# Performance work log

Hardware: AMD Instinct MI355X
Metric: run time of the kernel (lower is better)

The kernel has to match this reference:

```python
import jax, jax.numpy as jnp
import numpy as np

N, E, D, H, HOPS, HEAD_DIM = 50000, 800000, 256, 8, 2, 32


def setup_inputs() -> dict:
    key = jax.random.key(0)
    ks = jax.random.split(key, 9)
    scale = 1.0 / np.sqrt(D)  # mimic nn.Linear init scale
    return {
        "node_features": jax.random.normal(ks[0], (N, D), dtype=jnp.float32),
        "Wh_w": jax.random.normal(ks[1], (H, D, D), dtype=jnp.float32) * scale,
        "Wh_b": jax.random.normal(ks[2], (H, D), dtype=jnp.float32) * scale,
        "Wp_w": jax.random.normal(ks[3], (H, HEAD_DIM, D), dtype=jnp.float32) * scale,
        "Wp_b": jax.random.normal(ks[4], (H, HEAD_DIM), dtype=jnp.float32) * scale,
        "gate_vector": jax.random.normal(ks[5], (H,), dtype=jnp.float32),
        "hop_weights": jax.random.normal(ks[6], (HOPS,), dtype=jnp.float32),
        "src": jax.random.randint(ks[7], (E,), 0, N, dtype=jnp.int32),
        "dst": jax.random.randint(ks[8], (E,), 0, N, dtype=jnp.int32),
    }


def reference(node_features, Wh_w, Wh_b, Wp_w, Wp_b, gate_vector, hop_weights, src, dst):
    n = node_features.shape[0]
    num_heads = Wh_w.shape[0]
    num_hops = hop_weights.shape[0]

    # in-degree for mean reduce; zero-degree nodes aggregate to 0 (DGL default)
    deg = jax.ops.segment_sum(jnp.ones_like(dst, dtype=node_features.dtype), dst, num_segments=n)
    inv_deg = jnp.where(deg > 0, 1.0 / jnp.maximum(deg, 1.0), 0.0)[:, None]

    def aggregate(x):
        # per-head linear transform, gather src, mean-reduce per dst, then mean over heads
        acc = jnp.zeros_like(x)
        for h in range(num_heads):  # small fixed loop over structurally distinct heads
            ht = x @ Wh_w[h].T + Wh_b[h]                                  # (N, D)
            agg = jax.ops.segment_sum(ht[src], dst, num_segments=n) * inv_deg
            acc = acc + agg
        return acc / num_heads

    hop_w = jax.nn.softmax(hop_weights)
    cur = node_features
    h_fused = jnp.zeros_like(node_features)
    for k in range(num_hops):
        cur = aggregate(cur)
        h_fused = h_fused + hop_w[k] * cur

    # information perception: per-head projections gated by softmax, concatenated
    gates = jax.nn.softmax(gate_vector)
    z = jnp.einsum('nd,hod->nho', h_fused, Wp_w) + Wp_b[None]            # (N, H, head_dim)
    z = z * gates[None, :, None]
    return z.reshape(n, -1)                                               # (N, D)
```

## Files before the change

### kernel.cpp

```cpp
#include <hip/hip_runtime.h>
#include <math.h>

#define DFEAT 256

typedef short bf16x8 __attribute__((ext_vector_type(8)));
typedef float f32x4 __attribute__((ext_vector_type(4)));
typedef float f32x2 __attribute__((ext_vector_type(2)));

__device__ __forceinline__ unsigned short f2bf(float f) {
  union { float f; unsigned int u; } v;
  v.f = f;
  unsigned int r = v.u + 0x7fff + ((v.u >> 16) & 1);
  return (unsigned short)(r >> 16);
}

__device__ __forceinline__ uint2 pk_f8x8(const float* s) {
  int w0 = 0, w1 = 0;
  w0 = __builtin_amdgcn_cvt_pk_fp8_f32(s[0], s[1], w0, false);
  w0 = __builtin_amdgcn_cvt_pk_fp8_f32(s[2], s[3], w0, true);
  w1 = __builtin_amdgcn_cvt_pk_fp8_f32(s[4], s[5], w1, false);
  w1 = __builtin_amdgcn_cvt_pk_fp8_f32(s[6], s[7], w1, true);
  uint2 r; r.x = (unsigned)w0; r.y = (unsigned)w1;
  return r;
}

__device__ __forceinline__ int wave_incl_scan(int x, int lane) {
#pragma unroll
  for (int off = 1; off < 64; off <<= 1) {
    int t = __shfl_up(x, off);
    if (lane >= off) x += t;
  }
  return x;
}

__global__ void k_scan1(const int* __restrict__ deg, int N, int* __restrict__ bsum) {
  const int tid = threadIdx.x, lane = tid & 63, wave = tid >> 6;
  int i = blockIdx.x * 256 + tid;
  int v = (i < N) ? deg[i] : 0;
  int s = v;
#pragma unroll
  for (int off = 1; off < 64; off <<= 1) s += __shfl_xor(s, off);
  __shared__ int ws[4];
  if (lane == 0) ws[wave] = s;
  __syncthreads();
  if (tid == 0) bsum[blockIdx.x] = ws[0] + ws[1] + ws[2] + ws[3];
}

__global__ void k_scan2(int* __restrict__ bsum, int nb) {
  const int tid = threadIdx.x, lane = tid & 63, wave = tid >> 6;
  int v = (tid < nb) ? bsum[tid] : 0;
  int incl = wave_incl_scan(v, lane);
  __shared__ int ws[4];
  if (lane == 63) ws[wave] = incl;
  __syncthreads();
  int add = 0;
  for (int w = 0; w < wave; ++w) add += ws[w];
  if (tid < nb) bsum[tid] = add + incl - v;
}

__global__ void k_scan3(const int* __restrict__ deg, const int* __restrict__ bexcl, int N,
                        int* __restrict__ offs, int* __restrict__ cursor,
                        float* __restrict__ invd, float* __restrict__ mask,
                        unsigned char* __restrict__ maskb) {
  const int tid = threadIdx.x, lane = tid & 63, wave = tid >> 6;
  int i = blockIdx.x * 256 + tid;
  int v = (i < N) ? deg[i] : 0;
  int incl = wave_incl_scan(v, lane);
  __shared__ int ws[4];
  if (lane == 63) ws[wave] = incl;
  __syncthreads();
  int add = bexcl[blockIdx.x];
  for (int w = 0; w < wave; ++w) add += ws[w];
  if (i < N) {
    offs[i + 1] = add + incl;
    cursor[i] = add + incl - v;
    invd[i] = v > 0 ? 1.0f / (float)v : 0.0f;
    mask[i] = v > 0 ? 1.0f : 0.0f;
    maskb[i] = v > 0 ? 1 : 0;
  }
  if (i == 0) offs[0] = 0;
}

__global__ __launch_bounds__(256) void k_front(
    const int* __restrict__ dst, int E, int* __restrict__ deg,
    const float* __restrict__ x, int N, unsigned char* __restrict__ xi8,
    float* __restrict__ rscale,
    const float* __restrict__ Wh_w, const float* __restrict__ Wh_b, int H,
    const float* __restrict__ Wp_w, const float* __restrict__ Wp_b,
    const float* __restrict__ gate,
    float* __restrict__ Wbar, float* __restrict__ bbar,
    float* __restrict__ Wcat, float* __restrict__ bcat,
    int nDeg, int nQ) {
  const int bid = blockIdx.x;
  if (bid < nDeg) {
    int i = bid * 256 + threadIdx.x;
    if (i < E) atomicAdd(&deg[dst[i]], 1);
  } else if (bid < nDeg + nQ) {
    const int tid = threadIdx.x;
    const int wave = tid >> 6, half = (tid & 63) >> 5, l5 = tid & 31;
    const int row = (bid - nDeg) * 8 + wave * 2 + half;
    if (row < N) {
      const float4 v0 = *reinterpret_cast<const float4*>(x + (size_t)row * DFEAT + l5 * 8);
      const float4 v1 = *reinterpret_cast<const float4*>(x + (size_t)row * DFEAT + l5 * 8 + 4);
      float s[8] = {v0.x, v0.y, v0.z, v0.w, v1.x, v1.y, v1.z, v1.w};
      float mr = 0.f;
#pragma unroll
      for (int j = 0; j < 8; ++j) mr = fmaxf(mr, fabsf(s[j]));
#pragma unroll
      for (int off = 1; off < 32; off <<= 1) mr = fmaxf(mr, __shfl_xor(mr, off));
      const float qs = 127.0f / fmaxf(mr, 1e-20f);
      unsigned lo = 0, hi = 0;
#pragma unroll
      for (int j = 0; j < 4; ++j) {
        int q = (int)rintf(s[j] * qs);
        q = max(-127, min(127, q));
        lo |= ((unsigned)(unsigned char)(signed char)q) << (8 * j);
      }
#pragma unroll
      for (int j = 0; j < 4; ++j) {
        int q = (int)rintf(s[4 + j] * qs);
        q = max(-127, min(127, q));
        hi |= ((unsigned)(unsigned char)(signed char)q) << (8 * j);
      }
      uint2 r; r.x = lo; r.y = hi;
      *reinterpret_cast<uint2*>(xi8 + (size_t)row * DFEAT + l5 * 8) = r;
      if (l5 == 0) rscale[row] = mr * (1.0f / 127.0f);
    }
  } else {
    int j = (bid - nDeg - nQ) * 256 + threadIdx.x;
    float mx = -1e30f;
    for (int h = 0; h < H; ++h) mx = fmaxf(mx, gate[h]);
    float ssum = 0.f;
    for (int h = 0; h < H; ++h) ssum += expf(gate[h] - mx);
    const float inv = 1.0f / ssum;
    float s = 0.f;
    for (int h = 0; h < H; ++h) s += Wh_w[h * 65536 + j];
    Wbar[j] = s / (float)H;
    Wcat[j] = expf(gate[j >> 13] - mx) * inv * Wp_w[j];
    if (j < DFEAT) {
      float b = 0.f;
      for (int h = 0; h < H; ++h) b += Wh_b[h * DFEAT + j];
      bbar[j] = b / (float)H;
      bcat[j] = expf(gate[j >> 5] - mx) * inv * Wp_b[j];
    }
  }
}

__device__ __forceinline__ void mm_body(const float* __restrict__ A,
                                        const float* __restrict__ B,
                                        float* __restrict__ C, int i) {
  const int d = threadIdx.x;
  const float* Ar = A + i * DFEAT;
  float a0 = 0.f, a1 = 0.f, a2 = 0.f, a3 = 0.f, a4 = 0.f, a5 = 0.f, a6 = 0.f, a7 = 0.f;
  for (int k = 0; k < DFEAT; k += 8) {
    a0 = fmaf(Ar[k + 0], B[(k + 0) * DFEAT + d], a0);
    a1 = fmaf(Ar[k + 1], B[(k + 1) * DFEAT + d], a1);
    a2 = fmaf(Ar[k + 2], B[(k + 2) * DFEAT + d], a2);
    a3 = fmaf(Ar[k + 3], B[(k + 3) * DFEAT + d], a3);
    a4 = fmaf(Ar[k + 4], B[(k + 4) * DFEAT + d], a4);
    a5 = fmaf(Ar[k + 5], B[(k + 5) * DFEAT + d], a5);
    a6 = fmaf(Ar[k + 6], B[(k + 6) * DFEAT + d], a6);
    a7 = fmaf(Ar[k + 7], B[(k + 7) * DFEAT + d], a7);
  }
  C[i * DFEAT + d] = ((a0 + a1) + (a2 + a3)) + ((a4 + a5) + (a6 + a7));
}

__device__ __forceinline__ void bprep_body(int b, const float* __restrict__ W1,
                                           const float* __restrict__ W2,
                                           const float* __restrict__ Wcat,
                                           const float* __restrict__ bbar,
                                           const float* __restrict__ hopw,
                                           unsigned short* __restrict__ Bpk,
                                           float* __restrict__ c1s, float* __restrict__ c2s) {
  const float m2 = fmaxf(hopw[0], hopw[1]);
  const float e0 = expf(hopw[0] - m2), e1 = expf(hopw[1] - m2);
  const float hw0 = e0 / (e0 + e1), hw1 = e1 / (e0 + e1);
  if (b < 64) {
    int flat = b * 256 + threadIdx.x;
    int t = flat >> 10;
    int c = (flat >> 6) & 15;
    int chunk = flat & 63;
    int lr = chunk & 15;
    int lg = chunk >> 4;
    const float* W = (t < 8) ? W1 : W2;
    const float hw = (t < 8) ? hw0 : hw1;
    const float* p = W + (c * 16 + lr) * DFEAT + (t & 7) * 32 + lg * 8;
    unsigned short o[8];
#pragma unroll
    for (int j = 0; j < 8; ++j) o[j] = f2bf(hw * p[j]);
    ulonglong2* dstp = reinterpret_cast<ulonglong2*>(Bpk + (size_t)flat * 8);
    *dstp = *reinterpret_cast<ulonglong2*>(o);
  } else {
    int i = threadIdx.x;
    float s1 = 0.f, s2 = 0.f;
    for (int k = 0; k < DFEAT; ++k) {
      float bb = bbar[k];
      s1 = fmaf(Wcat[i * DFEAT + k], bb, s1);
      s2 = fmaf(W1[i * DFEAT + k], bb, s2);
    }
    c1s[i] = (hw0 + hw1) * s1;
    c2s[i] = hw1 * s2;
  }
}

__device__ __forceinline__ void acc8i8f(float* a, const uint2 q, const float rs) {
  a[0] = fmaf(rs, (float)(signed char)(q.x & 0xff), a[0]);
  a[1] = fmaf(rs, (float)(signed char)((q.x >> 8) & 0xff), a[1]);
  a[2] = fmaf(rs, (float)(signed char)((q.x >> 16) & 0xff), a[2]);
  a[3] = fmaf(rs, (float)(signed char)(q.x >> 24), a[3]);
  a[4] = fmaf(rs, (float)(signed char)(q.y & 0xff), a[4]);
  a[5] = fmaf(rs, (float)(signed char)((q.y >> 8) & 0xff), a[5]);
  a[6] = fmaf(rs, (float)(signed char)((q.y >> 16) & 0xff), a[6]);
  a[7] = fmaf(rs, (float)(signed char)(q.y >> 24), a[7]);
}
__device__ __forceinline__ void acc8f8(float* a, const uint2 q) {
  const f32x2 p0 = __builtin_amdgcn_cvt_pk_f32_fp8(q.x, false);
  const f32x2 p1 = __builtin_amdgcn_cvt_pk_f32_fp8(q.x, true);
  const f32x2 p2 = __builtin_amdgcn_cvt_pk_f32_fp8(q.y, false);
  const f32x2 p3 = __builtin_amdgcn_cvt_pk_f32_fp8(q.y, true);
  a[0] += p0[0]; a[1] += p0[1]; a[2] += p1[0]; a[3] += p1[1];
  a[4] += p2[0]; a[5] += p2[1]; a[6] += p3[0]; a[7] += p3[1];
}

__device__ __forceinline__ void agg1_body(int aggBlk,
                                          const unsigned char* __restrict__ xi8,
                                          const float* __restrict__ rscale,
                                          const int* __restrict__ csr,
                                          const int* __restrict__ offs,
                                          const float* __restrict__ invd, int N,
                                          unsigned short* __restrict__ m0bf,
                                          unsigned char* __restrict__ m0f8) {
  const int wid = (aggBlk * 256 + (int)threadIdx.x) >> 6;
  const int lane = threadIdx.x & 63;
  if (wid >= N) return;
  const int half = lane >> 5, l5 = lane & 31;
  const int beg = offs[wid];
  const int cnt = offs[wid + 1] - beg;
  float a[8] = {0.f, 0.f, 0.f, 0.f, 0.f, 0.f, 0.f, 0.f};

  for (int base = 0; base < cnt; base += 64) {
    const int m = min(64, cnt - base);
    int idx = 0;
    if (base + lane < cnt) idx = csr[beg + base + lane];
    int be = 0;
    for (; be + 8 <= m; be += 8) {
      int s[4];
#pragma unroll
      for (int k = 0; k < 4; ++k) s[k] = __shfl(idx, be + 2 * k + half);
      float rs[4];
#pragma unroll
      for (int k = 0; k < 4; ++k) rs[k] = rscale[s[k]];
      uint2 q[4];
#pragma unroll
      for (int k = 0; k < 4; ++k)
        q[k] = *reinterpret_cast<const uint2*>(xi8 + (size_t)s[k] * DFEAT + l5 * 8);
#pragma unroll
      for (int k = 0; k < 4; ++k) acc8i8f(a, q[k], rs[k]);
    }
    for (int e0 = be; e0 < m; e0 += 2) {
      const int e = e0 + half;
      const int s = __shfl(idx, (e < m) ? e : 0);
      if (e < m) {
        const float rs = rscale[s];
        const uint2 q = *reinterpret_cast<const uint2*>(xi8 + (size_t)s * DFEAT + l5 * 8);
        acc8i8f(a, q, rs);
      }
    }
  }
#pragma unroll
  for (int j = 0; j < 8; ++j) a[j] += __shfl_xor(a[j], 32);
  if (lane < 32) {
    const float w = invd[wid];
    float s[8];
#pragma unroll
    for (int j = 0; j < 8; ++j) s[j] = a[j] * w;
    uint4 r;
    r.x = (unsigned)f2bf(s[0]) | ((unsigned)f2bf(s[1]) << 16);
    r.y = (unsigned)f2bf(s[2]) | ((unsigned)f2bf(s[3]) << 16);
    r.z = (unsigned)f2bf(s[4]) | ((unsigned)f2bf(s[5]) << 16);
    r.w = (unsigned)f2bf(s[6]) | ((unsigned)f2bf(s[7]) << 16);
    *reinterpret_cast<uint4*>(m0bf + (size_t)wid * DFEAT + l5 * 8) = r;
    *reinterpret_cast<uint2*>(m0f8 + (size_t)wid * DFEAT + l5 * 8) = pk_f8x8(s);
  }
}

__device__ __forceinline__ void agg2_body(int aggBlk,
                                          const unsigned char* __restrict__ m0f8,
                                          const int* __restrict__ csr,
                                          const int* __restrict__ offs,
                                          const float* __restrict__ invd, int N,
                                          unsigned short* __restrict__ mm0bf,
                                          const unsigned char* __restrict__ maskb,
                                          float* __restrict__ f) {
  const int wid = (aggBlk * 256 + (int)threadIdx.x) >> 6;
  const int lane = threadIdx.x & 63;
  if (wid >= N) return;
  const int half = lane >> 5, l5 = lane & 31;
  const int beg = offs[wid];
  const int cnt = offs[wid + 1] - beg;
  float a[8] = {0.f, 0.f, 0.f, 0.f, 0.f, 0.f, 0.f, 0.f};
  float fm = 0.f;

  for (int base = 0; base < cnt; base += 64) {
    const int m = min(64, cnt - base);
    int idx = 0;
    if (base + lane < cnt) idx = csr[beg + base + lane];
    int be = 0;
    for (; be + 8 <= m; be += 8) {
      int s[4];
#pragma unroll
      for (int k = 0; k < 4; ++k) s[k] = __shfl(idx, be + 2 * k + half);
      uint2 q[4];
#pragma unroll
      for (int k = 0; k < 4; ++k)
        q[k] = *reinterpret_cast<const uint2*>(m0f8 + (size_t)s[k] * DFEAT + l5 * 8);
#pragma unroll
      for (int k = 0; k < 4; ++k) acc8f8(a, q[k]);
#pragma unroll
      for (int k = 0; k < 4; ++k) fm += (float)maskb[s[k]];
    }
    for (int e0 = be; e0 < m; e0 += 2) {
      const int e = e0 + half;
      const int s = __shfl(idx, (e < m) ? e : 0);
      if (e < m) {
        const uint2 q = *reinterpret_cast<const uint2*>(m0f8 + (size_t)s * DFEAT + l5 * 8);
        acc8f8(a, q);
        fm += (float)maskb[s];
      }
    }
  }
#pragma unroll
  for (int j = 0; j < 8; ++j) a[j] += __shfl_xor(a[j], 32);
  const float w = invd[wid];
  if (lane < 32) {
    float s[8];
#pragma unroll
    for (int j = 0; j < 8; ++j) s[j] = a[j] * w;
    uint4 r;
    r.x = (unsigned)f2bf(s[0]) | ((unsigned)f2bf(s[1]) << 16);
    r.y = (unsigned)f2bf(s[2]) | ((unsigned)f2bf(s[3]) << 16);
    r.z = (unsigned)f2bf(s[4]) | ((unsigned)f2bf(s[5]) << 16);
    r.w = (unsigned)f2bf(s[6]) | ((unsigned)f2bf(s[7]) << 16);
    *reinterpret_cast<uint4*>(mm0bf + (size_t)wid * DFEAT + l5 * 8) = r;
  }
  fm += __shfl_xor(fm, 32);
  if (lane == 0) f[wid] = fm * w;
}

__global__ __launch_bounds__(256) void k_fill_mm1(
    const int* __restrict__ src, const int* __restrict__ dst, int E,
    int* __restrict__ cursor, int* __restrict__ csr,
    const float* __restrict__ Wcat, const float* __restrict__ Wbar,
    float* __restrict__ W1) {
  if (blockIdx.x < 256) { mm_body(Wcat, Wbar, W1, blockIdx.x); return; }
  int i = (blockIdx.x - 256) * 256 + threadIdx.x;
  if (i < E) {
    int p = atomicAdd(&cursor[dst[i]], 1);
    csr[p] = src[i];
  }
}

__global__ __launch_bounds__(256) void k_agg1_mm2(
    const unsigned char* __restrict__ xi8, const float* __restrict__ rscale,
    const int* __restrict__ csr,
    const int* __restrict__ offs, const float* __restrict__ invd, int N,
    unsigned short* __restrict__ m0bf, unsigned char* __restrict__ m0f8,
    const float* __restrict__ W1, const float* __restrict__ Wbar,
    float* __restrict__ W2) {
  if (blockIdx.x < 256) { mm_body(W1, Wbar, W2, blockIdx.x); return; }
  agg1_body(blockIdx.x - 256, xi8, rscale, csr, offs, invd, N, m0bf, m0f8);
}

__global__ __launch_bounds__(256) void k_agg2_bprep(
    const unsigned char* __restrict__ m0f8, const int* __restrict__ csr,
    const int* __restrict__ offs, const float* __restrict__ invd, int N,
    unsigned short* __restrict__ mm0bf,
    const unsigned char* __restrict__ maskb, float* __restrict__ fbuf,
    const float* __restrict__ W1, const float* __restrict__ W2,
    const float* __restrict__ Wcat, const float* __restrict__ bbar,
    const float* __restrict__ hopw, unsigned short* __restrict__ Bpk,
    float* __restrict__ c1s, float* __restrict__ c2s) {
  if (blockIdx.x < 65) {
    bprep_body(blockIdx.x, W1, W2, Wcat, bbar, hopw, Bpk, c1s, c2s);
    return;
  }
  agg2_body(blockIdx.x - 65, m0f8, csr, offs, invd, N, mm0bf, maskb, fbuf);
}

__global__ __launch_bounds__(256, 2) void k_final_mfma(
    const unsigned short* __restrict__ m0bf, const unsigned short* __restrict__ mm0bf,
    const unsigned short* __restrict__ Bpk,
    const float* __restrict__ mask, const float* __restrict__ fbuf,
    const float* __restrict__ c1s, const float* __restrict__ c2s,
    const float* __restrict__ bcat, float* __restrict__ out, int N) {
  const int tid = threadIdx.x;
  const int lane = tid & 63;
  const int wave = tid >> 6;
  const int r0 = blockIdx.x * 128 + wave * 32;
  if (r0 >= N) return;
  const int lr = lane & 15;
  const int lg = lane >> 4;
  const uint4* Bv = reinterpret_cast<const uint4*>(Bpk);

  f32x4 acc[2][16];
#pragma unroll
  for (int fr = 0; fr < 2; ++fr)
#pragma unroll
    for (int c = 0; c < 16; ++c) acc[fr][c] = (f32x4){0.f, 0.f, 0.f, 0.f};

  const int arow0 = r0 + lr;
  const int arow1 = r0 + 16 + lr;
  const bool ok0 = arow0 < N, ok1 = arow1 < N;
  const size_t ab0 = (size_t)arow0 * DFEAT + lg * 8;
  const size_t ab1 = (size_t)arow1 * DFEAT + lg * 8;
  const bf16x8 zf = (bf16x8){0, 0, 0, 0, 0, 0, 0, 0};

  bf16x8 an0 = ok0 ? *reinterpret_cast<const bf16x8*>(m0bf + ab0) : zf;
  bf16x8 an1 = ok1 ? *reinterpret_cast<const bf16x8*>(m0bf + ab1) : zf;

  for (int t = 0; t < 16; ++t) {
    bf16x8 b[16];
#pragma unroll
    for (int c = 0; c < 16; ++c)
      b[c] = *reinterpret_cast<const bf16x8*>(&Bv[t * 1024 + c * 64 + lane]);
    const bf16x8 a0 = an0, a1 = an1;
    if (t < 15) {
      const unsigned short* As = (t + 1 < 8) ? m0bf : mm0bf;
      const int kb = ((t + 1) & 7) * 32;
      an0 = ok0 ? *reinterpret_cast<const bf16x8*>(As + ab0 + kb) : zf;
      an1 = ok1 ? *reinterpret_cast<const bf16x8*>(As + ab1 + kb) : zf;
    }
#pragma unroll
    for (int c = 0; c < 16; ++c) {
      acc[0][c] = __builtin_amdgcn_mfma_f32_16x16x32_bf16(a0, b[c], acc[0][c], 0, 0, 0);
      acc[1][c] = __builtin_amdgcn_mfma_f32_16x16x32_bf16(a1, b[c], acc[1][c], 0, 0, 0);
    }
  }

#pragma unroll
  for (int fr = 0; fr < 2; ++fr) {
    const int rbase = r0 + fr * 16 + lg * 4;
    float mk[4], fv[4];
#pragma unroll
    for (int i = 0; i < 4; ++i) {
      int r = rbase + i;
      mk[i] = (r < N) ? mask[r] : 0.f;
      fv[i] = (r < N) ? fbuf[r] : 0.f;
    }
#pragma unroll
    for (int c = 0; c < 16; ++c) {
      const int col = c * 16 + lr;
      const float c1 = c1s[col], c2 = c2s[col], bc = bcat[col];
#pragma unroll
      for (int i = 0; i < 4; ++i) {
        const int r = rbase + i;
        if (r < N) out[(size_t)r * DFEAT + col] = acc[fr][c][i] + mk[i] * c1 + fv[i] * c2 + bc;
      }
    }
  }
}

extern "C" void kernel_launch(void* const* d_in, const int* in_sizes, int n_in,
                              void* d_out, int out_size, void* d_ws, size_t ws_size,
                              hipStream_t stream) {
  const float* x    = (const float*)d_in[0];
  const float* Wh_w = (const float*)d_in[1];
  const float* Wh_b = (const float*)d_in[2];
  const float* Wp_w = (const float*)d_in[3];
  const float* Wp_b = (const float*)d_in[4];
  const float* gate = (const float*)d_in[5];
  const float* hopw = (const float*)d_in[6];
  const int* src    = (const int*)d_in[7];
  const int* dst    = (const int*)d_in[8];

  const int H = in_sizes[5];
  const int E = in_sizes[7];
  const int N = in_sizes[0] / DFEAT;
  float* out = (float*)d_out;

  char* w = (char*)d_ws;
  auto take = [&](size_t bytes) -> char* {
    char* p = w;
    w += (bytes + 255) & ~(size_t)255;
    return p;
  };
  unsigned char* xi8    = (unsigned char*)take((size_t)N * DFEAT);
  unsigned char* m0f8   = (unsigned char*)take((size_t)N * DFEAT);
  unsigned short* m0bf  = (unsigned short*)take((size_t)N * DFEAT * 2);
  unsigned short* mm0bf = (unsigned short*)take((size_t)N * DFEAT * 2);
  unsigned short* Bpk   = (unsigned short*)take((size_t)512 * 256 * 2);
  int* csr     = (int*)take((size_t)E * 4);
  int* offs    = (int*)take((size_t)(N + 1) * 4);
  int* cursor  = (int*)take((size_t)N * 4);
  int* deg     = (int*)take((size_t)N * 4);
  float* invd  = (float*)take((size_t)N * 4);
  float* mask  = (float*)take((size_t)N * 4);
  float* fbuf  = (float*)take((size_t)N * 4);
  float* rscale = (float*)take((size_t)N * 4);
  unsigned char* maskb = (unsigned char*)take((size_t)N);
  float* Wbar  = (float*)take(65536 * 4);
  float* Wcat  = (float*)take(65536 * 4);
  float* W1    = (float*)take(65536 * 4);
  float* W2    = (float*)take(65536 * 4);
  float* bbar  = (float*)take(256 * 4);
  float* bcat  = (float*)take(256 * 4);
  float* c1s   = (float*)take(256 * 4);
  float* c2s   = (float*)take(256 * 4);
  int* bsum    = (int*)take(256 * 4);

  const int nScanBlocks = (N + 255) / 256;
  const int nDeg = (E + 255) / 256;
  const int nQ = (N + 7) / 8;
  const int nFill = (E + 255) / 256;
  const int aggBlocks = (N + 3) / 4;

  hipMemsetAsync(deg, 0, (size_t)N * 4, stream);

  k_front<<<nDeg + nQ + 256, 256, 0, stream>>>(dst, E, deg, x, N, xi8, rscale,
                                               Wh_w, Wh_b, H, Wp_w, Wp_b, gate,
                                               Wbar, bbar, Wcat, bcat, nDeg, nQ);
  k_scan1<<<nScanBlocks, 256, 0, stream>>>(deg, N, bsum);
  k_scan2<<<1, 256, 0, stream>>>(bsum, nScanBlocks);
  k_scan3<<<nScanBlocks, 256, 0, stream>>>(deg, bsum, N, offs, cursor, invd, mask, maskb);

  k_fill_mm1<<<256 + nFill, 256, 0, stream>>>(src, dst, E, cursor, csr, Wcat, Wbar, W1);

  k_agg1_mm2<<<256 + aggBlocks, 256, 0, stream>>>(xi8, rscale, csr, offs, invd, N,
                                                  m0bf, m0f8, W1, Wbar, W2);
  k_agg2_bprep<<<65 + aggBlocks, 256, 0, stream>>>(m0f8, csr, offs, invd, N, mm0bf,
                                                   maskb, fbuf, W1, W2, Wcat, bbar,
                                                   hopw, Bpk, c1s, c2s);

  k_final_mfma<<<(N + 127) / 128, 256, 0, stream>>>(m0bf, mm0bf, Bpk, mask, fbuf,
                                                    c1s, c2s, bcat, out, N);
}
```

Before: 225.5 us.

## Split final MFMA GEMM columns across waves and double-buffer B/A fragment loads

The final GEMM kernel now gives each block 64 rows, with pairs of waves splitting the 256 output columns into two halves. This halves the accumulator and B-fragment register footprint per wave, and the launch bound is raised to 3 blocks per SM. The K loop is restructured into an explicit ping-pong over two B/A fragment buffers so the next tile's loads overlap the current MFMAs. Out-of-range rows are clamped instead of zero-masked, which trades per-block reuse of B across rows for higher occupancy and more blocks.

Result: slower. 232.9 us (+3.3%).

```diff
diff --git a/kernel.cpp b/kernel.cpp
--- a/kernel.cpp
+++ b/kernel.cpp
@@ -387,7 +387,7 @@
   agg2_body(blockIdx.x - 65, m0f8, csr, offs, invd, N, mm0bf, maskb, fbuf);
 }
 
-__global__ __launch_bounds__(256, 2) void k_final_mfma(
+__global__ __launch_bounds__(256, 3) void k_final_mfma(
     const unsigned short* __restrict__ m0bf, const unsigned short* __restrict__ mm0bf,
     const unsigned short* __restrict__ Bpk,
     const float* __restrict__ mask, const float* __restrict__ fbuf,
@@ -396,44 +396,66 @@
   const int tid = threadIdx.x;
   const int lane = tid & 63;
   const int wave = tid >> 6;
-  const int r0 = blockIdx.x * 128 + wave * 32;
+  const int rg = wave >> 1;
+  const int cg = wave & 1;
+  const int r0 = blockIdx.x * 64 + rg * 32;
   if (r0 >= N) return;
   const int lr = lane & 15;
   const int lg = lane >> 4;
   const uint4* Bv = reinterpret_cast<const uint4*>(Bpk);
-
-  f32x4 acc[2][16];
+  const int bbase = cg * 8 * 64 + lane;
+
+  f32x4 acc[2][8];
 #pragma unroll
   for (int fr = 0; fr < 2; ++fr)
 #pragma unroll
-    for (int c = 0; c < 16; ++c) acc[fr][c] = (f32x4){0.f, 0.f, 0.f, 0.f};
-
-  const int arow0 = r0 + lr;
-  const int arow1 = r0 + 16 + lr;
-  const bool ok0 = arow0 < N, ok1 = arow1 < N;
+    for (int c = 0; c < 8; ++c) acc[fr][c] = (f32x4){0.f, 0.f, 0.f, 0.f};
+
+  const int arow0 = min(r0 + lr, N - 1);
+  const int arow1 = min(r0 + 16 + lr, N - 1);
   const size_t ab0 = (size_t)arow0 * DFEAT + lg * 8;
   const size_t ab1 = (size_t)arow1 * DFEAT + lg * 8;
-  const bf16x8 zf = (bf16x8){0, 0, 0, 0, 0, 0, 0, 0};
-
-  bf16x8 an0 = ok0 ? *reinterpret_cast<const bf16x8*>(m0bf + ab0) : zf;
-  bf16x8 an1 = ok1 ? *reinterpret_cast<const bf16x8*>(m0bf + ab1) : zf;
-
-  for (int t = 0; t < 16; ++t) {
-    bf16x8 b[16];
-#pragma unroll
-    for (int c = 0; c < 16; ++c)
-      b[c] = *reinterpret_cast<const bf16x8*>(&Bv[t * 1024 + c * 64 + lane]);
-    const bf16x8 a0 = an0, a1 = an1;
-    if (t < 15) {
-      const unsigned short* As = (t + 1 < 8) ? m0bf : mm0bf;
-      const int kb = ((t + 1) & 7) * 32;
-      an0 = ok0 ? *reinterpret_cast<const bf16x8*>(As + ab0 + kb) : zf;
-      an1 = ok1 ? *reinterpret_cast<const bf16x8*>(As + ab1 + kb) : zf;
-    }
-#pragma unroll
-    for (int c = 0; c < 16; ++c) {
-      acc[0][c] = __builtin_amdgcn_mfma_f32_16x16x32_bf16(a0, b[c], acc[0][c], 0, 0, 0);
-      acc[1][c] = __builtin_amdgcn_mfma_f32_16x16x32_bf16(a1, b[c], acc[1][c], 0, 0, 0);
+
+  bf16x8 bA[8], bB[8];
+  bf16x8 ac0, ac1, an0, an1;
+#pragma unroll
+  for (int c = 0; c < 8; ++c)
+    bA[c] = *reinterpret_cast<const bf16x8*>(&Bv[bbase + c * 64]);
+  ac0 = *reinterpret_cast<const bf16x8*>(m0bf + ab0);
+  ac1 = *reinterpret_cast<const bf16x8*>(m0bf + ab1);
+
+  for (int tt = 0; tt < 16; tt += 2) {
+    {
+      const int tn = tt + 1;
+#pragma unroll
+      for (int c = 0; c < 8; ++c)
+        bB[c] = *reinterpret_cast<const bf16x8*>(&Bv[tn * 1024 + bbase + c * 64]);
+      const unsigned short* As = (tn < 8) ? m0bf : mm0bf;
+      const int kb = (tn & 7) * 32;
+      an0 = *reinterpret_cast<const bf16x8*>(As + ab0 + kb);
+      an1 = *reinterpret_cast<const bf16x8*>(As + ab1 + kb);
+#pragma unroll
+      for (int c = 0; c < 8; ++c) {
+        acc[0][c] = __builtin_amdgcn_mfma_f32_16x16x32_bf16(ac0, bA[c], acc[0][c], 0, 0, 0);
+        acc[1][c] = __builtin_amdgcn_mfma_f32_16x16x32_bf16(ac1, bA[c], acc[1][c], 0, 0, 0);
+      }
+    }
+    {
+      const int tn = tt + 2;
+      if (tn < 16) {
+#pragma unroll
+        for (int c = 0; c < 8; ++c)
+          bA[c] = *reinterpret_cast<const bf16x8*>(&Bv[tn * 1024 + bbase + c * 64]);
+        const unsigned short* As = (tn < 8) ? m0bf : mm0bf;
+        const int kb = (tn & 7) * 32;
+        ac0 = *reinterpret_cast<const bf16x8*>(As + ab0 + kb);
+        ac1 = *reinterpret_cast<const bf16x8*>(As + ab1 + kb);
+      }
+#pragma unroll
+      for (int c = 0; c < 8; ++c) {
+        acc[0][c] = __builtin_amdgcn_mfma_f32_16x16x32_bf16(an0, bB[c], acc[0][c], 0, 0, 0);
+        acc[1][c] = __builtin_amdgcn_mfma_f32_16x16x32_bf16(an1, bB[c], acc[1][c], 0, 0, 0);
+      }
     }
   }
 
@@ -448,8 +470,8 @@
       fv[i] = (r < N) ? fbuf[r] : 0.f;
     }
 #pragma unroll
-    for (int c = 0; c < 16; ++c) {
-      const int col = c * 16 + lr;
+    for (int c = 0; c < 8; ++c) {
+      const int col = cg * 128 + c * 16 + lr;
       const float c1 = c1s[col], c2 = c2s[col], bc = bcat[col];
 #pragma unroll
       for (int i = 0; i < 4; ++i) {
@@ -531,6 +553,6 @@
                                                    maskb, fbuf, W1, W2, Wcat, bbar,
                                                    hopw, Bpk, c1s, c2s);
 
-  k_final_mfma<<<(N + 127) / 128, 256, 0, stream>>>(m0bf, mm0bf, Bpk, mask, fbuf,
-                                                    c1s, c2s, bcat, out, N);
-}
+  k_final_mfma<<<(N + 63) / 64, 256, 0, stream>>>(m0bf, mm0bf, Bpk, mask, fbuf,
+                                                  c1s, c2s, bcat, out, N);
+}
```
